# Performance work log

Hardware: AMD Instinct MI355X
Metric: run time of the kernel (lower is better)

The kernel has to match this reference:

```python
import jax, jax.numpy as jnp
import numpy as np

D = 256  # input_dim
B = 2048

def setup_inputs() -> dict:
    key = jax.random.key(0)
    ks = jax.random.split(key, 6)
    x = jax.random.normal(ks[0], (B, D), dtype=jnp.float32)
    offsets = jax.random.normal(ks[1], (D,), dtype=jnp.float32)
    coeff0 = jax.random.normal(ks[2], (), dtype=jnp.float32)
    coeff1 = jax.random.normal(ks[3], (D,), dtype=jnp.float32)
    coeff2 = jax.random.normal(ks[4], (D, D), dtype=jnp.float32)
    coeff3 = jax.random.normal(ks[5], (D, D, D), dtype=jnp.float32)
    return {"x": x, "offsets": offsets, "coeff0": coeff0, "coeff1": coeff1,
            "coeff2": coeff2, "coeff3": coeff3}

def reference(x, offsets, coeff0, coeff1, coeff2, coeff3):
    # Truncated Taylor series around learned offsets: out[b] = c0 + sum_i <coeff_i, rel^{\otimes i}>[b]
    rel = x - offsets  # (B, D)
    out = coeff0  # scalar, broadcasts to (B,)
    for c in (coeff1, coeff2, coeff3):
        # contract one mode of the rank-i coefficient with rel at a time
        t = jnp.einsum('...d,bd->b...', c, rel)  # (B, D^{i-1})
        while t.ndim > 1:
            t = jnp.einsum('b...d,bd->b...', t, rel)
        out = out + t  # (B,)
    return out
```

## Files before the change

### kernel.cpp

```cpp
#include <hip/hip_runtime.h>
#include <hip/hip_bf16.h>

#define DD 256
#define BB 2048
#define BM 128
#define BN 64
#define NTILE ((DD * DD) / BM)
#define NSTAGE (BB / BN)

typedef __bf16 bf16x8 __attribute__((ext_vector_type(8)));
typedef float  f32x4  __attribute__((ext_vector_type(4)));

#define AS1 __attribute__((address_space(1)))
#define AS3 __attribute__((address_space(3)))

__device__ __forceinline__ unsigned short f2bf(float f) {
    unsigned int u = __float_as_uint(f);
    return (unsigned short)((u + 0x7FFFu + ((u >> 16) & 1u)) >> 16);
}
__device__ __forceinline__ float bf2f(unsigned short s) {
    return __uint_as_float(((unsigned int)s) << 16);
}
__device__ __forceinline__ void async_cp16(const void* g, void* l) {
    __builtin_amdgcn_global_load_lds((const AS1 unsigned int*)g,
                                     (AS3 unsigned int*)l, 16, 0, 0);
}

__global__ void prep_all(const float* __restrict__ x, const float* __restrict__ offsets,
                         const float* __restrict__ c0, const float* __restrict__ c1,
                         float* __restrict__ rel_f32, unsigned short* __restrict__ rel_bf16,
                         float* __restrict__ out) {
    const int tid = threadIdx.x, wave = tid >> 6, lane = tid & 63;
    const float4 o4  = *(const float4*)(offsets + lane * 4);
    const float4 c14 = *(const float4*)(c1 + lane * 4);
#pragma unroll
    for (int i = 0; i < 2; ++i) {
        const int b = blockIdx.x * 8 + wave * 2 + i;
        const float4 x4 = *(const float4*)(x + (size_t)b * DD + lane * 4);
        float4 r;
        r.x = x4.x - o4.x; r.y = x4.y - o4.y; r.z = x4.z - o4.z; r.w = x4.w - o4.w;
        *(float4*)(rel_f32 + (size_t)b * DD + lane * 4) = r;
        ushort4 rb;
        rb.x = f2bf(r.x); rb.y = f2bf(r.y); rb.z = f2bf(r.z); rb.w = f2bf(r.w);
        *(ushort4*)(rel_bf16 + (size_t)b * DD + lane * 4) = rb;
        float s = r.x * c14.x + r.y * c14.y + r.z * c14.z + r.w * c14.w;
        s += __shfl_xor(s, 1);  s += __shfl_xor(s, 2);  s += __shfl_xor(s, 4);
        s += __shfl_xor(s, 8);  s += __shfl_xor(s, 16); s += __shfl_xor(s, 32);
        if (lane == 0) out[b] = c0[0] + s;
    }
}

__global__ __launch_bounds__(256, 2) void taylor3(
    const float* __restrict__ c3, const float* __restrict__ c2,
    const float* __restrict__ rel_f32, const unsigned short* __restrict__ rel_bf16,
    float* __restrict__ partial)
{
    __shared__ unsigned short Bs[2][BN * DD];
    __shared__ float relI[BB];
    __shared__ float c2row[BM];
    __shared__ float colsum[2][4][BN];

    const int tile = blockIdx.x;
    const int i_t   = tile >> 1;
    const int jbase = (tile & 1) << 7;
    const int tid  = threadIdx.x;
    const int wave = tid >> 6;
    const int lane = tid & 63;
    const int wm = wave & 1, wk = wave >> 1;
    const int lrow = lane & 15, quad = lane >> 4;

#pragma unroll
    for (int k = 0; k < 8; ++k) {
        const int b = tid + k * 256;
        relI[b] = rel_f32[(size_t)b * DD + i_t];
    }
    if (tid < BM) c2row[tid] = c2[i_t * DD + jbase + tid];

    bf16x8 afr[4][4];
    {
        const float* abase = c3 + (size_t)tile * BM * DD;
#pragma unroll
        for (int mt = 0; mt < 4; ++mt) {
            const int row = wm * 64 + mt * 16 + lrow;
            const float* p = abase + (size_t)row * DD + wk * 128 + quad * 8;
#pragma unroll
            for (int ks = 0; ks < 4; ++ks) {
                float4 f0 = *(const float4*)(p + ks * 32);
                float4 f1 = *(const float4*)(p + ks * 32 + 4);
                union { unsigned short u[8]; bf16x8 v; } cv;
                cv.u[0] = f2bf(f0.x); cv.u[1] = f2bf(f0.y);
                cv.u[2] = f2bf(f0.z); cv.u[3] = f2bf(f0.w);
                cv.u[4] = f2bf(f1.x); cv.u[5] = f2bf(f1.y);
                cv.u[6] = f2bf(f1.z); cv.u[7] = f2bf(f1.w);
                afr[ks][mt] = cv.v;
            }
        }
    }

    auto stage = [&](int nb, int buf) {
        const int b0 = nb * BN;
#pragma unroll
        for (int c = 0; c < 8; ++c) {
            const int r0 = c * 8 + wave * 2;
            const int row = r0 + (lane >> 5);
            const int g = (lane & 31) ^ (row & 7);
            const unsigned short* src = rel_bf16 + (size_t)(b0 + row) * DD + g * 8;
            async_cp16(src, &Bs[buf][r0 * DD]);
        }
    };

    stage(0, 0);
    int prev_b0 = -1;

    for (int nb = 0; nb < NSTAGE; ++nb) {
        const int cur = nb & 1;
        const int b0 = nb * BN;
        __syncthreads();
        if (nb + 1 < NSTAGE) stage(nb + 1, cur ^ 1);

        if (prev_b0 >= 0 && tid < BN) {
            const float v = colsum[cur ^ 1][0][tid] + colsum[cur ^ 1][1][tid]
                          + colsum[cur ^ 1][2][tid] + colsum[cur ^ 1][3][tid];
            partial[(size_t)tile * BB + prev_b0 + tid] = relI[prev_b0 + tid] * v;
        }

        f32x4 acc[4][4];
#pragma unroll
        for (int mt = 0; mt < 4; ++mt)
#pragma unroll
            for (int nt = 0; nt < 4; ++nt)
                acc[mt][nt] = (f32x4){0.f, 0.f, 0.f, 0.f};

#pragma unroll
        for (int ks = 0; ks < 4; ++ks) {
            const int glog = wk * 16 + ks * 4 + quad;
            bf16x8 bfr[4];
#pragma unroll
            for (int nt = 0; nt < 4; ++nt) {
                const int col = nt * 16 + lrow;
                const int g = glog ^ (col & 7);
                bfr[nt] = *(const bf16x8*)(&Bs[cur][col * DD + g * 8]);
            }
#pragma unroll
            for (int mt = 0; mt < 4; ++mt)
#pragma unroll
                for (int nt = 0; nt < 4; ++nt)
                    acc[mt][nt] = __builtin_amdgcn_mfma_f32_16x16x32_bf16(
                        afr[ks][mt], bfr[nt], acc[mt][nt], 0, 0, 0);
        }

        float sv[4];
#pragma unroll
        for (int nt = 0; nt < 4; ++nt) {
            const int col = nt * 16 + lrow;
            float s = 0.f;
#pragma unroll
            for (int mt = 0; mt < 4; ++mt) {
                const int el = wm * 64 + mt * 16 + quad * 4;
                const int e  = jbase + el;
                const int g  = (e >> 3) ^ (col & 7);
                const ushort4 rj = *(const ushort4*)(&Bs[cur][col * DD + g * 8 + (e & 7)]);
                float c2x = 0.f, c2y = 0.f, c2z = 0.f, c2w = 0.f;
                if (wk == 0) {
                    const float4 c2r = *(const float4*)(&c2row[el]);
                    c2x = c2r.x; c2y = c2r.y; c2z = c2r.z; c2w = c2r.w;
                }
                s += (acc[mt][nt][0] + c2x) * bf2f(rj.x);
                s += (acc[mt][nt][1] + c2y) * bf2f(rj.y);
                s += (acc[mt][nt][2] + c2z) * bf2f(rj.z);
                s += (acc[mt][nt][3] + c2w) * bf2f(rj.w);
            }
            s += __shfl_xor(s, 16, 64);
            s += __shfl_xor(s, 32, 64);
            sv[nt] = s;
        }
        {
            const float v01 = (quad & 1) ? sv[1] : sv[0];
            const float v23 = (quad & 1) ? sv[3] : sv[2];
            colsum[cur][wave][lane] = (quad & 2) ? v23 : v01;
        }
        prev_b0 = b0;
    }
    __syncthreads();
    if (tid < BN) {
        const float v = colsum[1][0][tid] + colsum[1][1][tid]
                      + colsum[1][2][tid] + colsum[1][3][tid];
        partial[(size_t)tile * BB + prev_b0 + tid] = relI[prev_b0 + tid] * v;
    }
}

__global__ void reduce_partial(const float* __restrict__ partial, float* __restrict__ out) {
    __shared__ f32x4 red[256];
    const int t = threadIdx.x;
    const int g = blockIdx.x * 4 + (t & 3);
    const int slice = t >> 2;
    f32x4 s = (f32x4){0.f, 0.f, 0.f, 0.f};
    for (int r = slice * 8; r < slice * 8 + 8; ++r)
        s += *(const f32x4*)(partial + (size_t)r * BB + g * 4);
    red[t] = s; __syncthreads();
    if (t < 128) red[t] += red[t + 128]; __syncthreads();
    if (t < 64)  red[t] += red[t + 64];  __syncthreads();
    if (t < 32)  red[t] += red[t + 32];  __syncthreads();
    if (t < 16)  red[t] += red[t + 16];  __syncthreads();
    if (t < 8)   red[t] += red[t + 8];   __syncthreads();
    if (t < 4) {
        const f32x4 v = red[t] + red[t + 4];
        float4* op = (float4*)(out + (size_t)(blockIdx.x * 4 + t) * 4);
        float4 o = *op;
        o.x += v[0]; o.y += v[1]; o.z += v[2]; o.w += v[3];
        *op = o;
    }
}

extern "C" void kernel_launch(void* const* d_in, const int* in_sizes, int n_in,
                              void* d_out, int out_size, void* d_ws, size_t ws_size,
                              hipStream_t stream) {
    const float* x       = (const float*)d_in[0];
    const float* offsets = (const float*)d_in[1];
    const float* c0      = (const float*)d_in[2];
    const float* c1      = (const float*)d_in[3];
    const float* c2      = (const float*)d_in[4];
    const float* c3      = (const float*)d_in[5];
    float* out = (float*)d_out;

    char* ws = (char*)d_ws;
    float* rel_f32 = (float*)ws;
    unsigned short* rel_bf16 = (unsigned short*)(ws + (size_t)BB * DD * 4);
    float* partial = (float*)(ws + (size_t)BB * DD * 6);

    prep_all<<<BB / 8, 256, 0, stream>>>(x, offsets, c0, c1, rel_f32, rel_bf16, out);
    taylor3<<<NTILE, 256, 0, stream>>>(c3, c2, rel_f32, rel_bf16, partial);
    reduce_partial<<<128, 256, 0, stream>>>(partial, out);
}
```

Baseline: 189.4 us.

## Double taylor3 block to 512 threads and replace partial reduction with atomics

```diff
diff --git a/kernel.cpp b/kernel.cpp
--- a/kernel.cpp
+++ b/kernel.cpp
@@ -50,15 +50,14 @@
     }
 }
 
-__global__ __launch_bounds__(256, 2) void taylor3(
+__global__ __launch_bounds__(512, 4) void taylor3(
     const float* __restrict__ c3, const float* __restrict__ c2,
     const float* __restrict__ rel_f32, const unsigned short* __restrict__ rel_bf16,
-    float* __restrict__ partial)
+    float* __restrict__ out)
 {
     __shared__ unsigned short Bs[2][BN * DD];
     __shared__ float relI[BB];
-    __shared__ float c2row[BM];
-    __shared__ float colsum[2][4][BN];
+    __shared__ float colsum[2][8][BN];
 
     const int tile = blockIdx.x;
     const int i_t   = tile >> 1;
@@ -66,22 +65,30 @@
     const int tid  = threadIdx.x;
     const int wave = tid >> 6;
     const int lane = tid & 63;
-    const int wm = wave & 1, wk = wave >> 1;
+    const int wm = wave & 3, wk = wave >> 2;
     const int lrow = lane & 15, quad = lane >> 4;
 
 #pragma unroll
-    for (int k = 0; k < 8; ++k) {
-        const int b = tid + k * 256;
+    for (int k = 0; k < 4; ++k) {
+        const int b = tid + k * 512;
         relI[b] = rel_f32[(size_t)b * DD + i_t];
     }
-    if (tid < BM) c2row[tid] = c2[i_t * DD + jbase + tid];
-
-    bf16x8 afr[4][4];
+
+    f32x4 c2a[2];
+    if (wk == 0) {
+#pragma unroll
+        for (int mt = 0; mt < 2; ++mt) {
+            const float4 t = *(const float4*)(c2 + i_t * DD + jbase + wm * 32 + mt * 16 + quad * 4);
+            c2a[mt] = (f32x4){t.x, t.y, t.z, t.w};
+        }
+    }
+
+    bf16x8 afr[4][2];
     {
         const float* abase = c3 + (size_t)tile * BM * DD;
 #pragma unroll
-        for (int mt = 0; mt < 4; ++mt) {
-            const int row = wm * 64 + mt * 16 + lrow;
+        for (int mt = 0; mt < 2; ++mt) {
+            const int row = wm * 32 + mt * 16 + lrow;
             const float* p = abase + (size_t)row * DD + wk * 128 + quad * 8;
 #pragma unroll
             for (int ks = 0; ks < 4; ++ks) {
@@ -100,8 +107,8 @@
     auto stage = [&](int nb, int buf) {
         const int b0 = nb * BN;
 #pragma unroll
-        for (int c = 0; c < 8; ++c) {
-            const int r0 = c * 8 + wave * 2;
+        for (int c = 0; c < 4; ++c) {
+            const int r0 = c * 16 + wave * 2;
             const int row = r0 + (lane >> 5);
             const int g = (lane & 31) ^ (row & 7);
             const unsigned short* src = rel_bf16 + (size_t)(b0 + row) * DD + g * 8;
@@ -109,31 +116,24 @@
         }
     };
 
-    stage(0, 0);
-    int prev_b0 = -1;
-
-    for (int nb = 0; nb < NSTAGE; ++nb) {
-        const int cur = nb & 1;
+    auto body = [&](int nb, int cur) {
         const int b0 = nb * BN;
         __syncthreads();
         if (nb + 1 < NSTAGE) stage(nb + 1, cur ^ 1);
 
-        if (prev_b0 >= 0 && tid < BN) {
-            const float v = colsum[cur ^ 1][0][tid] + colsum[cur ^ 1][1][tid]
-                          + colsum[cur ^ 1][2][tid] + colsum[cur ^ 1][3][tid];
-            partial[(size_t)tile * BB + prev_b0 + tid] = relI[prev_b0 + tid] * v;
-        }
-
-        f32x4 acc[4][4];
-#pragma unroll
-        for (int mt = 0; mt < 4; ++mt)
-#pragma unroll
-            for (int nt = 0; nt < 4; ++nt)
-                acc[mt][nt] = (f32x4){0.f, 0.f, 0.f, 0.f};
-
-#pragma unroll
-        for (int ks = 0; ks < 4; ++ks) {
-            const int glog = wk * 16 + ks * 4 + quad;
+        if (nb > 0 && lane < 8) {
+            const int b = wave * 8 + lane;
+            const int pb0 = b0 - BN;
+            float v = colsum[cur ^ 1][0][b];
+#pragma unroll
+            for (int w = 1; w < 8; ++w) v += colsum[cur ^ 1][w][b];
+            atomicAdd(out + pb0 + b, relI[pb0 + b] * v);
+        }
+
+        f32x4 acc[2][4];
+
+        {
+            const int glog = wk * 16 + quad;
             bf16x8 bfr[4];
 #pragma unroll
             for (int nt = 0; nt < 4; ++nt) {
@@ -141,35 +141,56 @@
                 const int g = glog ^ (col & 7);
                 bfr[nt] = *(const bf16x8*)(&Bs[cur][col * DD + g * 8]);
             }
-#pragma unroll
-            for (int mt = 0; mt < 4; ++mt)
+            const f32x4 z4 = (f32x4){0.f, 0.f, 0.f, 0.f};
+#pragma unroll
+            for (int mt = 0; mt < 2; ++mt)
+#pragma unroll
+                for (int nt = 0; nt < 4; ++nt)
+                    acc[mt][nt] = __builtin_amdgcn_mfma_f32_16x16x32_bf16(
+                        afr[0][mt], bfr[nt], z4, 0, 0, 0);
+        }
+#pragma unroll
+        for (int ks = 1; ks < 4; ++ks) {
+            const int glog = wk * 16 + ks * 4 + quad;
+            bf16x8 bfr[4];
+#pragma unroll
+            for (int nt = 0; nt < 4; ++nt) {
+                const int col = nt * 16 + lrow;
+                const int g = glog ^ (col & 7);
+                bfr[nt] = *(const bf16x8*)(&Bs[cur][col * DD + g * 8]);
+            }
+#pragma unroll
+            for (int mt = 0; mt < 2; ++mt)
 #pragma unroll
                 for (int nt = 0; nt < 4; ++nt)
                     acc[mt][nt] = __builtin_amdgcn_mfma_f32_16x16x32_bf16(
                         afr[ks][mt], bfr[nt], acc[mt][nt], 0, 0, 0);
         }
 
+        if (wk == 0) {
+#pragma unroll
+            for (int mt = 0; mt < 2; ++mt)
+#pragma unroll
+                for (int nt = 0; nt < 4; ++nt)
+                    acc[mt][nt] += c2a[mt];
+        }
+
         float sv[4];
 #pragma unroll
         for (int nt = 0; nt < 4; ++nt) {
             const int col = nt * 16 + lrow;
-            float s = 0.f;
-#pragma unroll
-            for (int mt = 0; mt < 4; ++mt) {
-                const int el = wm * 64 + mt * 16 + quad * 4;
-                const int e  = jbase + el;
-                const int g  = (e >> 3) ^ (col & 7);
+            float sacc[2] = {0.f, 0.f};
+#pragma unroll
+            for (int mt = 0; mt < 2; ++mt) {
+                const int e = jbase + wm * 32 + mt * 16 + quad * 4;
+                const int g = (e >> 3) ^ (col & 7);
                 const ushort4 rj = *(const ushort4*)(&Bs[cur][col * DD + g * 8 + (e & 7)]);
-                float c2x = 0.f, c2y = 0.f, c2z = 0.f, c2w = 0.f;
-                if (wk == 0) {
-                    const float4 c2r = *(const float4*)(&c2row[el]);
-                    c2x = c2r.x; c2y = c2r.y; c2z = c2r.z; c2w = c2r.w;
-                }
-                s += (acc[mt][nt][0] + c2x) * bf2f(rj.x);
-                s += (acc[mt][nt][1] + c2y) * bf2f(rj.y);
-                s += (acc[mt][nt][2] + c2z) * bf2f(rj.z);
-                s += (acc[mt][nt][3] + c2w) * bf2f(rj.w);
-            }
+                sacc[mt] = fmaf(acc[mt][nt][0], bf2f(rj.x), sacc[mt]);
+                sacc[mt] = fmaf(acc[mt][nt][1], bf2f(rj.y), sacc[mt]);
+                sacc[mt] = fmaf(acc[mt][nt][2], bf2f(rj.z), sacc[mt]);
+                sacc[mt] = fmaf(acc[mt][nt][3], bf2f(rj.w), sacc[mt]);
+            }
+            float s = sacc[0] + sacc[1];
             s += __shfl_xor(s, 16, 64);
             s += __shfl_xor(s, 32, 64);
             sv[nt] = s;
@@ -179,36 +200,22 @@
             const float v23 = (quad & 1) ? sv[3] : sv[2];
             colsum[cur][wave][lane] = (quad & 2) ? v23 : v01;
         }
-        prev_b0 = b0;
-    }
+    };
+
+    stage(0, 0);
+    for (int nb = 0; nb < NSTAGE; nb += 2) {
+        body(nb, 0);
+        body(nb + 1, 1);
+    }
+
     __syncthreads();
-    if (tid < BN) {
-        const float v = colsum[1][0][tid] + colsum[1][1][tid]
-                      + colsum[1][2][tid] + colsum[1][3][tid];
-        partial[(size_t)tile * BB + prev_b0 + tid] = relI[prev_b0 + tid] * v;
-    }
-}
-
-__global__ void reduce_partial(const float* __restrict__ partial, float* __restrict__ out) {
-    __shared__ f32x4 red[256];
-    const int t = threadIdx.x;
-    const int g = blockIdx.x * 4 + (t & 3);
-    const int slice = t >> 2;
-    f32x4 s = (f32x4){0.f, 0.f, 0.f, 0.f};
-    for (int r = slice * 8; r < slice * 8 + 8; ++r)
-        s += *(const f32x4*)(partial + (size_t)r * BB + g * 4);
-    red[t] = s; __syncthreads();
-    if (t < 128) red[t] += red[t + 128]; __syncthreads();
-    if (t < 64)  red[t] += red[t + 64];  __syncthreads();
-    if (t < 32)  red[t] += red[t + 32];  __syncthreads();
-    if (t < 16)  red[t] += red[t + 16];  __syncthreads();
-    if (t < 8)   red[t] += red[t + 8];   __syncthreads();
-    if (t < 4) {
-        const f32x4 v = red[t] + red[t + 4];
-        float4* op = (float4*)(out + (size_t)(blockIdx.x * 4 + t) * 4);
-        float4 o = *op;
-        o.x += v[0]; o.y += v[1]; o.z += v[2]; o.w += v[3];
-        *op = o;
+    if (lane < 8) {
+        const int b = wave * 8 + lane;
+        const int pb0 = BB - BN;
+        float v = colsum[1][0][b];
+#pragma unroll
+        for (int w = 1; w < 8; ++w) v += colsum[1][w][b];
+        atomicAdd(out + pb0 + b, relI[pb0 + b] * v);
     }
 }
 
@@ -226,9 +233,7 @@
     char* ws = (char*)d_ws;
     float* rel_f32 = (float*)ws;
     unsigned short* rel_bf16 = (unsigned short*)(ws + (size_t)BB * DD * 4);
-    float* partial = (float*)(ws + (size_t)BB * DD * 6);
 
     prep_all<<<BB / 8, 256, 0, stream>>>(x, offsets, c0, c1, rel_f32, rel_bf16, out);
-    taylor3<<<NTILE, 256, 0, stream>>>(c3, c2, rel_f32, rel_bf16, partial);
-    reduce_partial<<<128, 256, 0, stream>>>(partial, out);
-}
+    taylor3<<<NTILE, 512, 0, stream>>>(c3, c2, rel_f32, rel_bf16, out);
+}
```

New measurement: 212.3 us. 1.12x slower.

## Split taylor3 columns across 8 waves and read transposed rel from global

Applied to the files above, without the earlier changes.

```diff
diff --git a/kernel.cpp b/kernel.cpp
--- a/kernel.cpp
+++ b/kernel.cpp
@@ -28,7 +28,7 @@
 
 __global__ void prep_all(const float* __restrict__ x, const float* __restrict__ offsets,
                          const float* __restrict__ c0, const float* __restrict__ c1,
-                         float* __restrict__ rel_f32, unsigned short* __restrict__ rel_bf16,
+                         unsigned short* __restrict__ rel_bf16, float* __restrict__ rel_T,
                          float* __restrict__ out) {
     const int tid = threadIdx.x, wave = tid >> 6, lane = tid & 63;
     const float4 o4  = *(const float4*)(offsets + lane * 4);
@@ -39,10 +39,13 @@
         const float4 x4 = *(const float4*)(x + (size_t)b * DD + lane * 4);
         float4 r;
         r.x = x4.x - o4.x; r.y = x4.y - o4.y; r.z = x4.z - o4.z; r.w = x4.w - o4.w;
-        *(float4*)(rel_f32 + (size_t)b * DD + lane * 4) = r;
         ushort4 rb;
         rb.x = f2bf(r.x); rb.y = f2bf(r.y); rb.z = f2bf(r.z); rb.w = f2bf(r.w);
         *(ushort4*)(rel_bf16 + (size_t)b * DD + lane * 4) = rb;
+        rel_T[(size_t)(lane * 4 + 0) * BB + b] = r.x;
+        rel_T[(size_t)(lane * 4 + 1) * BB + b] = r.y;
+        rel_T[(size_t)(lane * 4 + 2) * BB + b] = r.z;
+        rel_T[(size_t)(lane * 4 + 3) * BB + b] = r.w;
         float s = r.x * c14.x + r.y * c14.y + r.z * c14.z + r.w * c14.w;
         s += __shfl_xor(s, 1);  s += __shfl_xor(s, 2);  s += __shfl_xor(s, 4);
         s += __shfl_xor(s, 8);  s += __shfl_xor(s, 16); s += __shfl_xor(s, 32);
@@ -50,13 +53,12 @@
     }
 }
 
-__global__ __launch_bounds__(256, 2) void taylor3(
+__global__ __launch_bounds__(512, 4) void taylor3(
     const float* __restrict__ c3, const float* __restrict__ c2,
-    const float* __restrict__ rel_f32, const unsigned short* __restrict__ rel_bf16,
+    const float* __restrict__ rel_T, const unsigned short* __restrict__ rel_bf16,
     float* __restrict__ partial)
 {
     __shared__ unsigned short Bs[2][BN * DD];
-    __shared__ float relI[BB];
     __shared__ float c2row[BM];
     __shared__ float colsum[2][4][BN];
 
@@ -66,14 +68,9 @@
     const int tid  = threadIdx.x;
     const int wave = tid >> 6;
     const int lane = tid & 63;
-    const int wm = wave & 1, wk = wave >> 1;
+    const int wm = wave & 1, wk = (wave >> 1) & 1, wn = wave >> 2;
     const int lrow = lane & 15, quad = lane >> 4;
 
-#pragma unroll
-    for (int k = 0; k < 8; ++k) {
-        const int b = tid + k * 256;
-        relI[b] = rel_f32[(size_t)b * DD + i_t];
-    }
     if (tid < BM) c2row[tid] = c2[i_t * DD + jbase + tid];
 
     bf16x8 afr[4][4];
@@ -100,8 +97,8 @@
     auto stage = [&](int nb, int buf) {
         const int b0 = nb * BN;
 #pragma unroll
-        for (int c = 0; c < 8; ++c) {
-            const int r0 = c * 8 + wave * 2;
+        for (int c = 0; c < 4; ++c) {
+            const int r0 = c * 16 + wave * 2;
             const int row = r0 + (lane >> 5);
             const int g = (lane & 31) ^ (row & 7);
             const unsigned short* src = rel_bf16 + (size_t)(b0 + row) * DD + g * 8;
@@ -109,83 +106,108 @@
         }
     };
 
-    stage(0, 0);
-    int prev_b0 = -1;
-
-    for (int nb = 0; nb < NSTAGE; ++nb) {
-        const int cur = nb & 1;
+    const float* relTp = rel_T + (size_t)i_t * BB;
+
+    auto body = [&](int nb, int cur) {
         const int b0 = nb * BN;
         __syncthreads();
         if (nb + 1 < NSTAGE) stage(nb + 1, cur ^ 1);
 
-        if (prev_b0 >= 0 && tid < BN) {
-            const float v = colsum[cur ^ 1][0][tid] + colsum[cur ^ 1][1][tid]
-                          + colsum[cur ^ 1][2][tid] + colsum[cur ^ 1][3][tid];
-            partial[(size_t)tile * BB + prev_b0 + tid] = relI[prev_b0 + tid] * v;
-        }
-
-        f32x4 acc[4][4];
-#pragma unroll
-        for (int mt = 0; mt < 4; ++mt)
-#pragma unroll
-            for (int nt = 0; nt < 4; ++nt)
-                acc[mt][nt] = (f32x4){0.f, 0.f, 0.f, 0.f};
-
-#pragma unroll
-        for (int ks = 0; ks < 4; ++ks) {
-            const int glog = wk * 16 + ks * 4 + quad;
-            bf16x8 bfr[4];
-#pragma unroll
-            for (int nt = 0; nt < 4; ++nt) {
-                const int col = nt * 16 + lrow;
+        if (nb > 0 && lane < 8) {
+            const int b = wave * 8 + lane;
+            const int pb0 = b0 - BN;
+            const float v = colsum[cur ^ 1][0][b] + colsum[cur ^ 1][1][b]
+                          + colsum[cur ^ 1][2][b] + colsum[cur ^ 1][3][b];
+            partial[(size_t)tile * BB + pb0 + b] = relTp[pb0 + b] * v;
+        }
+
+        f32x4 acc[4][2];
+        __builtin_amdgcn_s_setprio(1);
+        {
+            const int glog = wk * 16 + quad;
+            bf16x8 bfr[2];
+#pragma unroll
+            for (int nt = 0; nt < 2; ++nt) {
+                const int col = wn * 32 + nt * 16 + lrow;
                 const int g = glog ^ (col & 7);
                 bfr[nt] = *(const bf16x8*)(&Bs[cur][col * DD + g * 8]);
             }
+            const f32x4 z4 = (f32x4){0.f, 0.f, 0.f, 0.f};
 #pragma unroll
             for (int mt = 0; mt < 4; ++mt)
 #pragma unroll
-                for (int nt = 0; nt < 4; ++nt)
+                for (int nt = 0; nt < 2; ++nt)
+                    acc[mt][nt] = __builtin_amdgcn_mfma_f32_16x16x32_bf16(
+                        afr[0][mt], bfr[nt], z4, 0, 0, 0);
+        }
+#pragma unroll
+        for (int ks = 1; ks < 4; ++ks) {
+            const int glog = wk * 16 + ks * 4 + quad;
+            bf16x8 bfr[2];
+#pragma unroll
+            for (int nt = 0; nt < 2; ++nt) {
+                const int col = wn * 32 + nt * 16 + lrow;
+                const int g = glog ^ (col & 7);
+                bfr[nt] = *(const bf16x8*)(&Bs[cur][col * DD + g * 8]);
+            }
+#pragma unroll
+            for (int mt = 0; mt < 4; ++mt)
+#pragma unroll
+                for (int nt = 0; nt < 2; ++nt)
                     acc[mt][nt] = __builtin_amdgcn_mfma_f32_16x16x32_bf16(
                         afr[ks][mt], bfr[nt], acc[mt][nt], 0, 0, 0);
         }
-
-        float sv[4];
-#pragma unroll
-        for (int nt = 0; nt < 4; ++nt) {
-            const int col = nt * 16 + lrow;
-            float s = 0.f;
+        __builtin_amdgcn_s_setprio(0);
+
+        if (wk == 0) {
 #pragma unroll
             for (int mt = 0; mt < 4; ++mt) {
-                const int el = wm * 64 + mt * 16 + quad * 4;
-                const int e  = jbase + el;
-                const int g  = (e >> 3) ^ (col & 7);
+                const float4 c2r = *(const float4*)(&c2row[wm * 64 + mt * 16 + quad * 4]);
+                const f32x4 c2v = (f32x4){c2r.x, c2r.y, c2r.z, c2r.w};
+#pragma unroll
+                for (int nt = 0; nt < 2; ++nt)
+                    acc[mt][nt] += c2v;
+            }
+        }
+
+        float sv[2];
+#pragma unroll
+        for (int nt = 0; nt < 2; ++nt) {
+            const int col = wn * 32 + nt * 16 + lrow;
+            float s0 = 0.f, s1 = 0.f;
+#pragma unroll
+            for (int mt = 0; mt < 4; ++mt) {
+                const int e = jbase + wm * 64 + mt * 16 + quad * 4;
+                const int g = (e >> 3) ^ (col & 7);
                 const ushort4 rj = *(const ushort4*)(&Bs[cur][col * DD + g * 8 + (e & 7)]);
-                float c2x = 0.f, c2y = 0.f, c2z = 0.f, c2w = 0.f;
-                if (wk == 0) {
-                    const float4 c2r = *(const float4*)(&c2row[el]);
-                    c2x = c2r.x; c2y = c2r.y; c2z = c2r.z; c2w = c2r.w;
-                }
-                s += (acc[mt][nt][0] + c2x) * bf2f(rj.x);
-                s += (acc[mt][nt][1] + c2y) * bf2f(rj.y);
-                s += (acc[mt][nt][2] + c2z) * bf2f(rj.z);
-                s += (acc[mt][nt][3] + c2w) * bf2f(rj.w);
-            }
+                float& sa = (mt & 1) ? s1 : s0;
+                sa = fmaf(acc[mt][nt][0], bf2f(rj.x), sa);
+                sa = fmaf(acc[mt][nt][1], bf2f(rj.y), sa);
+                sa = fmaf(acc[mt][nt][2], bf2f(rj.z), sa);
+                sa = fmaf(acc[mt][nt][3], bf2f(rj.w), sa);
+            }
+            float s = s0 + s1;
             s += __shfl_xor(s, 16, 64);
             s += __shfl_xor(s, 32, 64);
             sv[nt] = s;
         }
-        {
-            const float v01 = (quad & 1) ? sv[1] : sv[0];
-            const float v23 = (quad & 1) ? sv[3] : sv[2];
-            colsum[cur][wave][lane] = (quad & 2) ? v23 : v01;
-        }
-        prev_b0 = b0;
-    }
+        if (lane < 32)
+            colsum[cur][wk * 2 + wm][wn * 32 + lane] = (lane & 16) ? sv[1] : sv[0];
+    };
+
+    stage(0, 0);
+    for (int nb = 0; nb < NSTAGE; nb += 2) {
+        body(nb, 0);
+        body(nb + 1, 1);
+    }
+
     __syncthreads();
-    if (tid < BN) {
-        const float v = colsum[1][0][tid] + colsum[1][1][tid]
-                      + colsum[1][2][tid] + colsum[1][3][tid];
-        partial[(size_t)tile * BB + prev_b0 + tid] = relI[prev_b0 + tid] * v;
+    if (lane < 8) {
+        const int b = wave * 8 + lane;
+        const int pb0 = BB - BN;
+        const float v = colsum[1][0][b] + colsum[1][1][b]
+                      + colsum[1][2][b] + colsum[1][3][b];
+        partial[(size_t)tile * BB + pb0 + b] = relTp[pb0 + b] * v;
     }
 }
 
@@ -224,11 +246,11 @@
     float* out = (float*)d_out;
 
     char* ws = (char*)d_ws;
-    float* rel_f32 = (float*)ws;
-    unsigned short* rel_bf16 = (unsigned short*)(ws + (size_t)BB * DD * 4);
-    float* partial = (float*)(ws + (size_t)BB * DD * 6);
-
-    prep_all<<<BB / 8, 256, 0, stream>>>(x, offsets, c0, c1, rel_f32, rel_bf16, out);
-    taylor3<<<NTILE, 256, 0, stream>>>(c3, c2, rel_f32, rel_bf16, partial);
+    unsigned short* rel_bf16 = (unsigned short*)ws;
+    float* rel_T   = (float*)(ws + (size_t)1 * 1024 * 1024);
+    float* partial = (float*)(ws + (size_t)3 * 1024 * 1024);
+
+    prep_all<<<BB / 8, 256, 0, stream>>>(x, offsets, c0, c1, rel_bf16, rel_T, out);
+    taylor3<<<NTILE, 512, 0, stream>>>(c3, c2, rel_T, rel_bf16, partial);
     reduce_partial<<<128, 256, 0, stream>>>(partial, out);
 }
```

New measurement: 256.2 us. 35.3% more time.
